# Optimization experiments

Measured on AMD Instinct MI355X. Metric: run time of the kernel, lower is better.

## Reference

```python
import jax, jax.numpy as jnp
import numpy as np

NODELEN = 394
N_NODES = 50000
N_EDGES = 200000
IN_DIM = 2 * NODELEN  # 788
H2 = 192
EMB = 128


def setup_inputs() -> dict:
    key = jax.random.key(0)
    ks = jax.random.split(key, 12)
    inp = {
        'features': jax.random.normal(ks[0], (N_NODES, NODELEN), dtype=jnp.float32),
        'src': jax.random.randint(ks[1], (N_EDGES,), 0, N_NODES),
        'dst': jax.random.randint(ks[2], (N_EDGES,), 0, N_NODES),
        # AutoEncoder params (Linear weights stored as [in, out])
        'W_enc1': jax.random.normal(ks[3], (IN_DIM, H2), dtype=jnp.float32) / np.sqrt(IN_DIM),
        'b_enc1': jnp.zeros((H2,), dtype=jnp.float32),
        'W_enc3': jax.random.normal(ks[4], (H2, EMB), dtype=jnp.float32) / np.sqrt(H2),
        'b_enc3': jnp.zeros((EMB,), dtype=jnp.float32),
        'W_dec1': jax.random.normal(ks[5], (EMB, H2), dtype=jnp.float32) / np.sqrt(EMB),
        'b_dec1': jnp.zeros((H2,), dtype=jnp.float32),
        'W_dec3': jax.random.normal(ks[6], (H2, IN_DIM), dtype=jnp.float32) / np.sqrt(H2),
        'b_dec3': jnp.zeros((IN_DIM,), dtype=jnp.float32),
    }
    return inp


def _segment_mean(msgs, dst, inv_deg, n):
    # msgs: [E, F] gathered neighbor features; mean over incoming edges per node
    return jax.ops.segment_sum(msgs, dst, num_segments=n) * inv_deg


def reference(features, src, dst, W_enc1, b_enc1, W_enc3, b_enc3,
              W_dec1, b_dec1, W_dec3, b_dec3):
    n = features.shape[0]
    ones = jnp.ones(src.shape[0], dtype=features.dtype)
    deg = jax.ops.segment_sum(ones, dst, num_segments=n)
    # nodes with no neighbors fall back to the zero dummy vector (as in source)
    inv_deg = (1.0 / jnp.maximum(deg, 1.0))[:, None]

    # depth-1 aggregation: mean of raw neighbor features, then feat[0] := 0
    h1 = _segment_mean(features[src], dst, inv_deg, n)
    h1 = h1.at[:, 0].set(0.0)
    # depth-2 aggregation: mean of depth-1 aggregates of neighbors, feat[0] := 0
    h2 = _segment_mean(h1[src], dst, inv_deg, n)
    h2 = h2.at[:, 0].set(0.0)

    # concatenated embedding with positions 0 and NODELEN zeroed
    emb = jnp.concatenate([features, h2], axis=1)  # [N, 788]
    emb = emb.at[:, 0].set(0.0).at[:, NODELEN].set(0.0)

    # AutoEncoder forward (dropout is identity at inference)
    x = jax.nn.relu(emb @ W_enc1 + b_enc1)
    encoded = x @ W_enc3 + b_enc3
    y = jax.nn.relu(encoded @ W_dec1 + b_dec1)
    decoded = y @ W_dec3 + b_dec3
    return encoded, decoded, emb
```

## Files before the change

### kernel.cpp

```cpp
#include <hip/hip_runtime.h>
#include <hip/hip_bf16.h>

#define NODELEN 394
#define IN_DIM 788
#define H2DIM 192
#define EMBDIM 128
#define NCHUNK 197

typedef __attribute__((ext_vector_type(4))) float f32x4;
typedef __attribute__((ext_vector_type(8))) short bfrag;

static __device__ __forceinline__ unsigned short f2bf(float f) {
    union { float f; unsigned u; } v; v.f = f;
    unsigned r = v.u + 0x7FFFu + ((v.u >> 16) & 1u);
    return (unsigned short)(r >> 16);
}
static __device__ __forceinline__ float bf2f(unsigned short h) {
    union { unsigned u; float f; } v; v.u = ((unsigned)h) << 16;
    return v.f;
}


__global__ void count_deg(const int* __restrict__ dst, int* __restrict__ deg, int e) {
    int i = blockIdx.x * blockDim.x + threadIdx.x;
    if (i < e) atomicAdd(&deg[dst[i]], 1);
}

__global__ void block_sum(const int* __restrict__ deg, int* __restrict__ bsum, int n) {
    __shared__ int s[256];
    int t = threadIdx.x;
    int i = blockIdx.x * 256 + t;
    s[t] = (i < n) ? deg[i] : 0;
    __syncthreads();
    for (int d = 128; d > 0; d >>= 1) {
        if (t < d) s[t] += s[t + d];
        __syncthreads();
    }
    if (t == 0) bsum[blockIdx.x] = s[0];
}

__global__ void scan_bsums(int* bsum, int nb) {
    __shared__ int s[256];
    int t = threadIdx.x;
    int x0 = (t < nb) ? bsum[t] : 0;
    s[t] = x0;
    __syncthreads();
    for (int d = 1; d < 256; d <<= 1) {
        int u = (t >= d) ? s[t - d] : 0;
        __syncthreads();
        s[t] += u;
        __syncthreads();
    }
    if (t < nb) bsum[t] = s[t] - x0;
}

__global__ void block_scan(const int* __restrict__ deg, const int* __restrict__ boff,
                           int* __restrict__ rowstart, int* __restrict__ cursor,
                           float* __restrict__ inv, int n) {
    __shared__ int s[256];
    int t = threadIdx.x;
    int i = blockIdx.x * 256 + t;
    int x0 = (i < n) ? deg[i] : 0;
    s[t] = x0;
    __syncthreads();
    for (int d = 1; d < 256; d <<= 1) {
        int u = (t >= d) ? s[t - d] : 0;
        __syncthreads();
        s[t] += u;
        __syncthreads();
    }
    if (i < n) {
        int r = boff[blockIdx.x] + s[t] - x0;
        rowstart[i] = r;
        cursor[i] = r;
        inv[i] = 1.0f / fmaxf((float)x0, 1.0f);
    }
}

__global__ void fill_edges(const int* __restrict__ src, const int* __restrict__ dst,
                           int* __restrict__ cursor, int* __restrict__ elist, int e) {
    int i = blockIdx.x * blockDim.x + threadIdx.x;
    if (i < e) {
        int p = atomicAdd(&cursor[dst[i]], 1);
        elist[p] = src[i];
    }
}


__global__ __launch_bounds__(256) void gather1(
        const float* __restrict__ feat, const int* __restrict__ rowstart,
        const int* __restrict__ deg, const float* __restrict__ inv,
        const int* __restrict__ elist, unsigned short* __restrict__ h1) {
    const int node = blockIdx.x;
    const int c = threadIdx.x;
    if (c >= NCHUNK) return;
    const int beg = rowstart[node];
    const int dc = deg[node];
    const float s = inv[node];
    const size_t off = (size_t)c * 2;

    float ax = 0.f, ay = 0.f, bx = 0.f, by = 0.f;
    float cx = 0.f, cy = 0.f, dx = 0.f, dy = 0.f;
    int j = 0;
    for (; j + 3 < dc; j += 4) {
        int n0 = elist[beg + j], n1 = elist[beg + j + 1];
        int n2 = elist[beg + j + 2], n3 = elist[beg + j + 3];
        float2 v0 = *(const float2*)(feat + (size_t)n0 * NODELEN + off);
        float2 v1 = *(const float2*)(feat + (size_t)n1 * NODELEN + off);
        float2 v2 = *(const float2*)(feat + (size_t)n2 * NODELEN + off);
        float2 v3 = *(const float2*)(feat + (size_t)n3 * NODELEN + off);
        ax += v0.x; ay += v0.y; bx += v1.x; by += v1.y;
        cx += v2.x; cy += v2.y; dx += v3.x; dy += v3.y;
    }
    for (; j < dc; ++j) {
        int n0 = elist[beg + j];
        float2 v0 = *(const float2*)(feat + (size_t)n0 * NODELEN + off);
        ax += v0.x; ay += v0.y;
    }
    float fx = (ax + bx + cx + dx) * s;
    float fy = (ay + by + cy + dy) * s;
    if (c == 0) fx = 0.f;
    unsigned out = ((unsigned)f2bf(fy) << 16) | (unsigned)f2bf(fx);
    *(unsigned*)(h1 + (size_t)node * NODELEN + off) = out;
}

__global__ __launch_bounds__(256) void gather2_emb(
        const float* __restrict__ feat, const unsigned* __restrict__ h1,
        const int* __restrict__ rowstart, const int* __restrict__ deg,
        const float* __restrict__ inv, const int* __restrict__ elist,
        float* __restrict__ emb) {
    const int node = blockIdx.x;
    const int c = threadIdx.x;
    if (c >= NCHUNK) return;
    const int beg = rowstart[node];
    const int dc = deg[node];
    const float s = inv[node];

    float ax = 0.f, ay = 0.f, bx = 0.f, by = 0.f;
    float cx = 0.f, cy = 0.f, dx = 0.f, dy = 0.f;
    int j = 0;
    for (; j + 3 < dc; j += 4) {
        int n0 = elist[beg + j], n1 = elist[beg + j + 1];
        int n2 = elist[beg + j + 2], n3 = elist[beg + j + 3];
        unsigned u0 = h1[(size_t)n0 * NCHUNK + c];
        unsigned u1 = h1[(size_t)n1 * NCHUNK + c];
        unsigned u2 = h1[(size_t)n2 * NCHUNK + c];
        unsigned u3 = h1[(size_t)n3 * NCHUNK + c];
        ax += bf2f((unsigned short)u0); ay += bf2f((unsigned short)(u0 >> 16));
        bx += bf2f((unsigned short)u1); by += bf2f((unsigned short)(u1 >> 16));
        cx += bf2f((unsigned short)u2); cy += bf2f((unsigned short)(u2 >> 16));
        dx += bf2f((unsigned short)u3); dy += bf2f((unsigned short)(u3 >> 16));
    }
    for (; j < dc; ++j) {
        int n0 = elist[beg + j];
        unsigned u0 = h1[(size_t)n0 * NCHUNK + c];
        ax += bf2f((unsigned short)u0); ay += bf2f((unsigned short)(u0 >> 16));
    }
    float hx = (ax + bx + cx + dx) * s;
    float hy = (ay + by + cy + dy) * s;

    const float* fr = feat + (size_t)node * NODELEN;
    float* er = emb + (size_t)node * IN_DIM;
    float2 fv = *(const float2*)(fr + c * 2);
    if (c == 0) { fv.x = 0.f; hx = 0.f; }
    *(float2*)(er + c * 2) = fv;
    float2 hv; hv.x = hx; hv.y = hy;
    *(float2*)(er + NODELEN + c * 2) = hv;
}

__device__ __forceinline__ void tr_one(const float* W, unsigned short* Wt,
                                       int K, int N, int Kp, int idx) {
    int nrow = idx / Kp, k = idx - nrow * Kp;
    Wt[idx] = (k < K) ? f2bf(W[(size_t)k * N + nrow]) : (unsigned short)0;
}

#define T1E (192 * 800)
#define T2E (128 * 192)
#define T3E (192 * 128)
#define T4E (788 * 192)

__global__ void transpose_all(const float* __restrict__ W1, unsigned short* __restrict__ Wt1,
                              const float* __restrict__ W2, unsigned short* __restrict__ Wt2,
                              const float* __restrict__ W3, unsigned short* __restrict__ Wt3,
                              const float* __restrict__ W4, unsigned short* __restrict__ Wt4) {
    int idx = blockIdx.x * 256 + threadIdx.x;
    if (idx < T1E) { tr_one(W1, Wt1, IN_DIM, H2DIM, 800, idx); return; }
    idx -= T1E;
    if (idx < T2E) { tr_one(W2, Wt2, H2DIM, EMBDIM, 192, idx); return; }
    idx -= T2E;
    if (idx < T3E) { tr_one(W3, Wt3, EMBDIM, H2DIM, 128, idx); return; }
    idx -= T3E;
    if (idx < T4E) { tr_one(W4, Wt4, H2DIM, IN_DIM, 192, idx); return; }
}

static __device__ __forceinline__ int bs_addr(int r, int s) {
    return r * 32 + ((s ^ ((r >> 1) & 3)) << 3);
}
static __device__ __forceinline__ int xy_base(int r, int s) {
    int ph = (s & 24) | ((s ^ r) & 7);
    return r * 192 + (ph << 3);
}
static __device__ __forceinline__ int xy_addr_s(int r, int col) { return xy_base(r, col >> 3) + (col & 7); }
static __device__ __forceinline__ int en_base(int r, int s) {
    int ph = (s & 8) | ((s ^ r) & 7);
    return r * 128 + (ph << 3);
}
static __device__ __forceinline__ int en_addr_s(int r, int col) { return en_base(r, col >> 3) + (col & 7); }

static __device__ __forceinline__ unsigned short f2bf_fast(float f) {
    __hip_bfloat16 h = __float2bfloat16(f);
    union { __hip_bfloat16 h; unsigned short u; } c; c.h = h; return c.u;
}

struct A8 { float4 a, b; };

static __device__ __forceinline__ void load_a(A8 out[2], const float* __restrict__ emb,
                                              int m0, int wm, int lr, int lk, int M, int kt) {
    int c = kt * 32 + lk * 8;
    #pragma unroll
    for (int i = 0; i < 2; ++i) {
        int gm = m0 + wm * 32 + i * 16 + lr;
        const float* rp = emb + (size_t)gm * IN_DIM;
        bool v = gm < M;
        if (v && c + 8 <= IN_DIM) {
            out[i].a = *(const float4*)(rp + c);
            out[i].b = *(const float4*)(rp + c + 4);
        } else {
            float t[8];
            #pragma unroll
            for (int q = 0; q < 8; ++q) t[q] = (v && c + q < IN_DIM) ? rp[c + q] : 0.f;
            out[i].a = make_float4(t[0], t[1], t[2], t[3]);
            out[i].b = make_float4(t[4], t[5], t[6], t[7]);
        }
    }
}

static __device__ __forceinline__ bfrag cvt_a(const A8& x) {
    union { unsigned short u[8]; bfrag v; } pk;
    pk.u[0] = f2bf_fast(x.a.x); pk.u[1] = f2bf_fast(x.a.y);
    pk.u[2] = f2bf_fast(x.a.z); pk.u[3] = f2bf_fast(x.a.w);
    pk.u[4] = f2bf_fast(x.b.x); pk.u[5] = f2bf_fast(x.b.y);
    pk.u[6] = f2bf_fast(x.b.z); pk.u[7] = f2bf_fast(x.b.w);
    return pk.v;
}

__global__ __launch_bounds__(256, 3) void mlp_fused(
    const float* __restrict__ emb,
    const unsigned short* __restrict__ Wt1,
    const unsigned short* __restrict__ Wt2,
    const unsigned short* __restrict__ Wt3,
    const unsigned short* __restrict__ Wt4,
    const float* __restrict__ b1, const float* __restrict__ b2,
    const float* __restrict__ b3, const float* __restrict__ b4,
    float* __restrict__ encoded, float* __restrict__ decoded, int M)
{
    __shared__ unsigned short Bs[192 * 32];
    __shared__ unsigned short XY[64 * 192];
    __shared__ unsigned short EN[64 * 128];

    const int tid = threadIdx.x;
    const int wid = tid >> 6, l = tid & 63;
    const int wm = wid >> 1, wn = wid & 1;
    const int lr = l & 15, lk = l >> 4;
    const int m0 = blockIdx.x * 64;
    const bfrag zf = {0, 0, 0, 0, 0, 0, 0, 0};

    const int r0 = tid >> 2, s0 = tid & 3;
    const int r1 = (tid + 256) >> 2;
    const int r2 = (tid + 512) >> 2;
    const int bw0 = bs_addr(r0, s0);
    const int bw1 = bs_addr(r1, s0);
    const int bw2 = bs_addr(r2, s0);
    int brd6[6], brd4[4];
    #pragma unroll
    for (int j = 0; j < 6; ++j) brd6[j] = bs_addr(wn * 96 + j * 16 + lr, lk);
    #pragma unroll
    for (int j = 0; j < 4; ++j) brd4[j] = bs_addr(wn * 64 + j * 16 + lr, lk);

    {
        f32x4 acc1[2][6];
        #pragma unroll
        for (int i = 0; i < 2; ++i)
            #pragma unroll
            for (int j = 0; j < 6; ++j) acc1[i][j] = (f32x4){0.f, 0.f, 0.f, 0.f};

        A8 aC[2], aN[2];
        bfrag bC[3], bN[3];
        load_a(aC, emb, m0, wm, lr, lk, M, 0);
        bC[0] = *(const bfrag*)(Wt1 + (size_t)r0 * 800 + s0 * 8);
        bC[1] = *(const bfrag*)(Wt1 + (size_t)r1 * 800 + s0 * 8);
        bC[2] = *(const bfrag*)(Wt1 + (size_t)r2 * 800 + s0 * 8);

        #pragma unroll 5
        for (int kt = 0; kt < 25; ++kt) {
            *(bfrag*)&Bs[bw0] = bC[0];
            *(bfrag*)&Bs[bw1] = bC[1];
            *(bfrag*)&Bs[bw2] = bC[2];
            if (kt < 24) {
                int k0 = (kt + 1) * 32;
                load_a(aN, emb, m0, wm, lr, lk, M, kt + 1);
                bN[0] = *(const bfrag*)(Wt1 + (size_t)r0 * 800 + k0 + s0 * 8);
                bN[1] = *(const bfrag*)(Wt1 + (size_t)r1 * 800 + k0 + s0 * 8);
                bN[2] = *(const bfrag*)(Wt1 + (size_t)r2 * 800 + k0 + s0 * 8);
            }
            __syncthreads();
            bfrag af0 = cvt_a(aC[0]), af1 = cvt_a(aC[1]);
            bfrag bf[6];
            #pragma unroll
            for (int j = 0; j < 6; ++j) bf[j] = *(const bfrag*)&Bs[brd6[j]];
            #pragma unroll
            for (int j = 0; j < 6; ++j) {
                acc1[0][j] = __builtin_amdgcn_mfma_f32_16x16x32_bf16(af0, bf[j], acc1[0][j], 0, 0, 0);
                acc1[1][j] = __builtin_amdgcn_mfma_f32_16x16x32_bf16(af1, bf[j], acc1[1][j], 0, 0, 0);
            }
            __syncthreads();
            if (kt < 24) {
                aC[0] = aN[0]; aC[1] = aN[1];
                bC[0] = bN[0]; bC[1] = bN[1]; bC[2] = bN[2];
            }
        }

        float bv[6];
        #pragma unroll
        for (int j = 0; j < 6; ++j) bv[j] = b1[wn * 96 + j * 16 + lr];
        #pragma unroll
        for (int i = 0; i < 2; ++i)
            #pragma unroll
            for (int j = 0; j < 6; ++j)
                #pragma unroll
                for (int r = 0; r < 4; ++r) {
                    int m = wm * 32 + i * 16 + lk * 4 + r;
                    int n1 = wn * 96 + j * 16 + lr;
                    XY[xy_addr_s(m, n1)] = f2bf_fast(fmaxf(acc1[i][j][r] + bv[j], 0.f));
                }
    }

    bfrag c3[3], n3[3];
    {
        bfrag c2[2], n2[2];
        c2[0] = *(const bfrag*)(Wt2 + (size_t)r0 * 192 + s0 * 8);
        c2[1] = *(const bfrag*)(Wt2 + (size_t)r1 * 192 + s0 * 8);
        f32x4 acc2[2][4];
        #pragma unroll
        for (int i = 0; i < 2; ++i)
            #pragma unroll
            for (int j = 0; j < 4; ++j) acc2[i][j] = (f32x4){0.f, 0.f, 0.f, 0.f};

        #pragma unroll
        for (int kt = 0; kt < 6; ++kt) {
            *(bfrag*)&Bs[bw0] = c2[0];
            *(bfrag*)&Bs[bw1] = c2[1];
            if (kt < 5) {
                int k0 = (kt + 1) * 32;
                n2[0] = *(const bfrag*)(Wt2 + (size_t)r0 * 192 + k0 + s0 * 8);
                n2[1] = *(const bfrag*)(Wt2 + (size_t)r1 * 192 + k0 + s0 * 8);
            } else {
                c3[0] = *(const bfrag*)(Wt3 + (size_t)r0 * 128 + s0 * 8);
                c3[1] = *(const bfrag*)(Wt3 + (size_t)r1 * 128 + s0 * 8);
                c3[2] = *(const bfrag*)(Wt3 + (size_t)r2 * 128 + s0 * 8);
            }
            __syncthreads();
            bfrag af[2];
            #pragma unroll
            for (int i = 0; i < 2; ++i)
                af[i] = *(const bfrag*)&XY[xy_base(wm * 32 + i * 16 + lr, kt * 4 + lk)];
            bfrag bf[4];
            #pragma unroll
            for (int j = 0; j < 4; ++j) bf[j] = *(const bfrag*)&Bs[brd4[j]];
            #pragma unroll
            for (int i = 0; i < 2; ++i)
                #pragma unroll
                for (int j = 0; j < 4; ++j)
                    acc2[i][j] = __builtin_amdgcn_mfma_f32_16x16x32_bf16(af[i], bf[j], acc2[i][j], 0, 0, 0);
            __syncthreads();
            if (kt < 5) { c2[0] = n2[0]; c2[1] = n2[1]; }
        }

        float bv[4];
        #pragma unroll
        for (int j = 0; j < 4; ++j) bv[j] = b2[wn * 64 + j * 16 + lr];
        #pragma unroll
        for (int i = 0; i < 2; ++i)
            #pragma unroll
            for (int j = 0; j < 4; ++j)
                #pragma unroll
                for (int r = 0; r < 4; ++r) {
                    int m = wm * 32 + i * 16 + lk * 4 + r;
                    int nn = wn * 64 + j * 16 + lr;
                    float v = acc2[i][j][r] + bv[j];
                    int gm = m0 + m;
                    if (gm < M) encoded[(size_t)gm * EMBDIM + nn] = v;
                    EN[en_addr_s(m, nn)] = f2bf_fast(v);
                }
    }

    bfrag c4[2], n4[2];
    {
        f32x4 acc3[2][6];
        #pragma unroll
        for (int i = 0; i < 2; ++i)
            #pragma unroll
            for (int j = 0; j < 6; ++j) acc3[i][j] = (f32x4){0.f, 0.f, 0.f, 0.f};

        #pragma unroll
        for (int kt = 0; kt < 4; ++kt) {
            *(bfrag*)&Bs[bw0] = c3[0];
            *(bfrag*)&Bs[bw1] = c3[1];
            *(bfrag*)&Bs[bw2] = c3[2];
            if (kt < 3) {
                int k0 = (kt + 1) * 32;
                n3[0] = *(const bfrag*)(Wt3 + (size_t)r0 * 128 + k0 + s0 * 8);
                n3[1] = *(const bfrag*)(Wt3 + (size_t)r1 * 128 + k0 + s0 * 8);
                n3[2] = *(const bfrag*)(Wt3 + (size_t)r2 * 128 + k0 + s0 * 8);
            } else {
                c4[0] = *(const bfrag*)(Wt4 + (size_t)r0 * 192 + s0 * 8);
                c4[1] = *(const bfrag*)(Wt4 + (size_t)r1 * 192 + s0 * 8);
            }
            __syncthreads();
            bfrag af[2];
            #pragma unroll
            for (int i = 0; i < 2; ++i)
                af[i] = *(const bfrag*)&EN[en_base(wm * 32 + i * 16 + lr, kt * 4 + lk)];
            bfrag bf[6];
            #pragma unroll
            for (int j = 0; j < 6; ++j) bf[j] = *(const bfrag*)&Bs[brd6[j]];
            #pragma unroll
            for (int i = 0; i < 2; ++i)
                #pragma unroll
                for (int j = 0; j < 6; ++j)
                    acc3[i][j] = __builtin_amdgcn_mfma_f32_16x16x32_bf16(af[i], bf[j], acc3[i][j], 0, 0, 0);
            __syncthreads();
            if (kt < 3) { c3[0] = n3[0]; c3[1] = n3[1]; c3[2] = n3[2]; }
        }

        float bv[6];
        #pragma unroll
        for (int j = 0; j < 6; ++j) bv[j] = b3[wn * 96 + j * 16 + lr];
        #pragma unroll
        for (int i = 0; i < 2; ++i)
            #pragma unroll
            for (int j = 0; j < 6; ++j)
                #pragma unroll
                for (int r = 0; r < 4; ++r) {
                    int m = wm * 32 + i * 16 + lk * 4 + r;
                    int n3c = wn * 96 + j * 16 + lr;
                    XY[xy_addr_s(m, n3c)] = f2bf_fast(fmaxf(acc3[i][j][r] + bv[j], 0.f));
                }
    }

    {
        bfrag af4[6][2];
        for (int nc = 0; nc < 7; ++nc) {
            f32x4 acc4[2][4];
            #pragma unroll
            for (int i = 0; i < 2; ++i)
                #pragma unroll
                for (int j = 0; j < 4; ++j) acc4[i][j] = (f32x4){0.f, 0.f, 0.f, 0.f};

            #pragma unroll
            for (int kt = 0; kt < 6; ++kt) {
                *(bfrag*)&Bs[bw0] = c4[0];
                *(bfrag*)&Bs[bw1] = c4[1];
                {
                    int nn = (kt < 5) ? nc : nc + 1;
                    int nk = (kt < 5) ? (kt + 1) * 32 : 0;
                    if (nn < 7) {
                        int g0 = nn * 128 + r0, g1 = nn * 128 + r1;
                        n4[0] = (g0 < IN_DIM) ? *(const bfrag*)(Wt4 + (size_t)g0 * 192 + nk + s0 * 8) : zf;
                        n4[1] = (g1 < IN_DIM) ? *(const bfrag*)(Wt4 + (size_t)g1 * 192 + nk + s0 * 8) : zf;
                    }
                }
                __syncthreads();
                if (nc == 0 && kt == 0) {
                    #pragma unroll
                    for (int q = 0; q < 6; ++q)
                        #pragma unroll
                        for (int i = 0; i < 2; ++i)
                            af4[q][i] = *(const bfrag*)&XY[xy_base(wm * 32 + i * 16 + lr, q * 4 + lk)];
                }
                bfrag bf[4];
                #pragma unroll
                for (int j = 0; j < 4; ++j) bf[j] = *(const bfrag*)&Bs[brd4[j]];
                #pragma unroll
                for (int i = 0; i < 2; ++i)
                    #pragma unroll
                    for (int j = 0; j < 4; ++j)
                        acc4[i][j] = __builtin_amdgcn_mfma_f32_16x16x32_bf16(af4[kt][i], bf[j], acc4[i][j], 0, 0, 0);
                __syncthreads();
                c4[0] = n4[0]; c4[1] = n4[1];
            }

            float bv[4];
            #pragma unroll
            for (int j = 0; j < 4; ++j) {
                int nn = nc * 128 + wn * 64 + j * 16 + lr;
                bv[j] = (nn < IN_DIM) ? b4[nn] : 0.f;
            }
            #pragma unroll
            for (int i = 0; i < 2; ++i)
                #pragma unroll
                for (int j = 0; j < 4; ++j)
                    #pragma unroll
                    for (int r = 0; r < 4; ++r) {
                        int gm = m0 + wm * 32 + i * 16 + lk * 4 + r;
                        int nn = nc * 128 + wn * 64 + j * 16 + lr;
                        if (gm < M && nn < IN_DIM)
                            decoded[(size_t)gm * IN_DIM + nn] = acc4[i][j][r] + bv[j];
                    }
        }
    }
}


extern "C" void kernel_launch(void* const* d_in, const int* in_sizes, int n_in,
                              void* d_out, int out_size, void* d_ws, size_t ws_size,
                              hipStream_t stream) {
    const float* features = (const float*)d_in[0];
    const int*   src      = (const int*)d_in[1];
    const int*   dst      = (const int*)d_in[2];
    const float* W_enc1   = (const float*)d_in[3];
    const float* b_enc1   = (const float*)d_in[4];
    const float* W_enc3   = (const float*)d_in[5];
    const float* b_enc3   = (const float*)d_in[6];
    const float* W_dec1   = (const float*)d_in[7];
    const float* b_dec1   = (const float*)d_in[8];
    const float* W_dec3   = (const float*)d_in[9];
    const float* b_dec3   = (const float*)d_in[10];

    const int n = in_sizes[0] / NODELEN;
    const int e = in_sizes[1];

    float* encoded = (float*)d_out;
    float* decoded = encoded + (size_t)n * EMBDIM;
    float* emb     = decoded + (size_t)n * IN_DIM;

    char* ws = (char*)d_ws;
    unsigned short* h1  = (unsigned short*)(ws + 0);
    unsigned short* Wt1 = (unsigned short*)(ws + 40000000);
    unsigned short* Wt2 = (unsigned short*)(ws + 40400000);
    unsigned short* Wt3 = (unsigned short*)(ws + 40500000);
    unsigned short* Wt4 = (unsigned short*)(ws + 40600000);
    float* inv          = (float*)(ws + 41000000);
    int*   deg          = (int*)  (ws + 41200000);
    int*   rowstart     = (int*)  (ws + 41400000);
    int*   cursor       = (int*)  (ws + 41600000);
    int*   elist        = (int*)  (ws + 41800000);
    int*   bsum         = (int*)  (ws + 42600000);

    const int nb = (n + 255) / 256;
    const int eb = (e + 255) / 256;

    transpose_all<<<(T1E + T2E + T3E + T4E + 255) / 256, 256, 0, stream>>>(
        W_enc1, Wt1, W_enc3, Wt2, W_dec1, Wt3, W_dec3, Wt4);

    hipMemsetAsync(deg, 0, (size_t)n * sizeof(int), stream);
    count_deg<<<eb, 256, 0, stream>>>(dst, deg, e);
    block_sum<<<nb, 256, 0, stream>>>(deg, bsum, n);
    scan_bsums<<<1, 256, 0, stream>>>(bsum, nb);
    block_scan<<<nb, 256, 0, stream>>>(deg, bsum, rowstart, cursor, inv, n);
    fill_edges<<<eb, 256, 0, stream>>>(src, dst, cursor, elist, e);

    gather1<<<n, 256, 0, stream>>>(features, rowstart, deg, inv, elist, h1);
    gather2_emb<<<n, 256, 0, stream>>>(features, (const unsigned*)h1, rowstart, deg,
                                       inv, elist, emb);

    const int MB = (n + 63) / 64;
    mlp_fused<<<MB, 256, 0, stream>>>(emb, Wt1, Wt2, Wt3, Wt4,
                                      b_enc1, b_enc3, b_dec1, b_dec3,
                                      encoded, decoded, n);
}
```

Baseline: 353.1 us.

## Load MLP weight fragments directly from global memory instead of staging through LDS

Removes the shared-memory B tile and its double-buffered register prefetch in all four GEMM stages. Each wave now reads its MFMA B fragments straight from global (L2-resident) weights and preloads the A fragments from XY/EN once per stage. This drops most __syncthreads and the LDS write/read round trip and frees LDS for occupancy. In exchange, the prefetch that hid global latency is gone, and each of the two wave rows in a block fetches the same weight data, raising L1/L2 traffic.

```diff
diff --git a/kernel.cpp b/kernel.cpp
--- a/kernel.cpp
+++ b/kernel.cpp
@@ -193,9 +193,6 @@
     if (idx < T4E) { tr_one(W4, Wt4, H2DIM, IN_DIM, 192, idx); return; }
 }
 
-static __device__ __forceinline__ int bs_addr(int r, int s) {
-    return r * 32 + ((s ^ ((r >> 1) & 3)) << 3);
-}
 static __device__ __forceinline__ int xy_base(int r, int s) {
     int ph = (s & 24) | ((s ^ r) & 7);
     return r * 192 + (ph << 3);
@@ -254,7 +251,6 @@
     const float* __restrict__ b3, const float* __restrict__ b4,
     float* __restrict__ encoded, float* __restrict__ decoded, int M)
 {
-    __shared__ unsigned short Bs[192 * 32];
     __shared__ unsigned short XY[64 * 192];
     __shared__ unsigned short EN[64 * 128];
 
@@ -265,61 +261,32 @@
     const int m0 = blockIdx.x * 64;
     const bfrag zf = {0, 0, 0, 0, 0, 0, 0, 0};
 
-    const int r0 = tid >> 2, s0 = tid & 3;
-    const int r1 = (tid + 256) >> 2;
-    const int r2 = (tid + 512) >> 2;
-    const int bw0 = bs_addr(r0, s0);
-    const int bw1 = bs_addr(r1, s0);
-    const int bw2 = bs_addr(r2, s0);
-    int brd6[6], brd4[4];
-    #pragma unroll
-    for (int j = 0; j < 6; ++j) brd6[j] = bs_addr(wn * 96 + j * 16 + lr, lk);
-    #pragma unroll
-    for (int j = 0; j < 4; ++j) brd4[j] = bs_addr(wn * 64 + j * 16 + lr, lk);
-
     {
-        f32x4 acc1[2][6];
+        f32x4 acc[2][6];
         #pragma unroll
         for (int i = 0; i < 2; ++i)
             #pragma unroll
-            for (int j = 0; j < 6; ++j) acc1[i][j] = (f32x4){0.f, 0.f, 0.f, 0.f};
-
-        A8 aC[2], aN[2];
-        bfrag bC[3], bN[3];
-        load_a(aC, emb, m0, wm, lr, lk, M, 0);
-        bC[0] = *(const bfrag*)(Wt1 + (size_t)r0 * 800 + s0 * 8);
-        bC[1] = *(const bfrag*)(Wt1 + (size_t)r1 * 800 + s0 * 8);
-        bC[2] = *(const bfrag*)(Wt1 + (size_t)r2 * 800 + s0 * 8);
+            for (int j = 0; j < 6; ++j) acc[i][j] = (f32x4){0.f, 0.f, 0.f, 0.f};
+
+        const unsigned short* wp[6];
+        #pragma unroll
+        for (int j = 0; j < 6; ++j)
+            wp[j] = Wt1 + (size_t)(wn * 96 + j * 16 + lr) * 800 + lk * 8;
 
         #pragma unroll 5
         for (int kt = 0; kt < 25; ++kt) {
-            *(bfrag*)&Bs[bw0] = bC[0];
-            *(bfrag*)&Bs[bw1] = bC[1];
-            *(bfrag*)&Bs[bw2] = bC[2];
-            if (kt < 24) {
-                int k0 = (kt + 1) * 32;
-                load_a(aN, emb, m0, wm, lr, lk, M, kt + 1);
-                bN[0] = *(const bfrag*)(Wt1 + (size_t)r0 * 800 + k0 + s0 * 8);
-                bN[1] = *(const bfrag*)(Wt1 + (size_t)r1 * 800 + k0 + s0 * 8);
-                bN[2] = *(const bfrag*)(Wt1 + (size_t)r2 * 800 + k0 + s0 * 8);
-            }
-            __syncthreads();
-            bfrag af0 = cvt_a(aC[0]), af1 = cvt_a(aC[1]);
+            A8 a[2];
+            load_a(a, emb, m0, wm, lr, lk, M, kt);
             bfrag bf[6];
             #pragma unroll
-            for (int j = 0; j < 6; ++j) bf[j] = *(const bfrag*)&Bs[brd6[j]];
+            for (int j = 0; j < 6; ++j) bf[j] = *(const bfrag*)(wp[j] + kt * 32);
+            bfrag af0 = cvt_a(a[0]), af1 = cvt_a(a[1]);
             #pragma unroll
             for (int j = 0; j < 6; ++j) {
-                acc1[0][j] = __builtin_amdgcn_mfma_f32_16x16x32_bf16(af0, bf[j], acc1[0][j], 0, 0, 0);
-                acc1[1][j] = __builtin_amdgcn_mfma_f32_16x16x32_bf16(af1, bf[j], acc1[1][j], 0, 0, 0);
-            }
-            __syncthreads();
-            if (kt < 24) {
-                aC[0] = aN[0]; aC[1] = aN[1];
-                bC[0] = bN[0]; bC[1] = bN[1]; bC[2] = bN[2];
+                acc[0][j] = __builtin_amdgcn_mfma_f32_16x16x32_bf16(af0, bf[j], acc[0][j], 0, 0, 0);
+                acc[1][j] = __builtin_amdgcn_mfma_f32_16x16x32_bf16(af1, bf[j], acc[1][j], 0, 0, 0);
             }
         }
-
         float bv[6];
         #pragma unroll
         for (int j = 0; j < 6; ++j) bv[j] = b1[wn * 96 + j * 16 + lr];
@@ -331,51 +298,41 @@
                 for (int r = 0; r < 4; ++r) {
                     int m = wm * 32 + i * 16 + lk * 4 + r;
                     int n1 = wn * 96 + j * 16 + lr;
-                    XY[xy_addr_s(m, n1)] = f2bf_fast(fmaxf(acc1[i][j][r] + bv[j], 0.f));
+                    XY[xy_addr_s(m, n1)] = f2bf_fast(fmaxf(acc[i][j][r] + bv[j], 0.f));
                 }
     }
-
-    bfrag c3[3], n3[3];
+    __syncthreads();
+
     {
-        bfrag c2[2], n2[2];
-        c2[0] = *(const bfrag*)(Wt2 + (size_t)r0 * 192 + s0 * 8);
-        c2[1] = *(const bfrag*)(Wt2 + (size_t)r1 * 192 + s0 * 8);
-        f32x4 acc2[2][4];
+        bfrag af2[6][2];
+        #pragma unroll
+        for (int q = 0; q < 6; ++q)
+            #pragma unroll
+            for (int i = 0; i < 2; ++i)
+                af2[q][i] = *(const bfrag*)&XY[xy_base(wm * 32 + i * 16 + lr, q * 4 + lk)];
+
+        f32x4 acc[2][4];
         #pragma unroll
         for (int i = 0; i < 2; ++i)
             #pragma unroll
-            for (int j = 0; j < 4; ++j) acc2[i][j] = (f32x4){0.f, 0.f, 0.f, 0.f};
+            for (int j = 0; j < 4; ++j) acc[i][j] = (f32x4){0.f, 0.f, 0.f, 0.f};
+
+        const unsigned short* wp[4];
+        #pragma unroll
+        for (int j = 0; j < 4; ++j)
+            wp[j] = Wt2 + (size_t)(wn * 64 + j * 16 + lr) * 192 + lk * 8;
 
         #pragma unroll
         for (int kt = 0; kt < 6; ++kt) {
-            *(bfrag*)&Bs[bw0] = c2[0];
-            *(bfrag*)&Bs[bw1] = c2[1];
-            if (kt < 5) {
-                int k0 = (kt + 1) * 32;
-                n2[0] = *(const bfrag*)(Wt2 + (size_t)r0 * 192 + k0 + s0 * 8);
-                n2[1] = *(const bfrag*)(Wt2 + (size_t)r1 * 192 + k0 + s0 * 8);
-            } else {
-                c3[0] = *(const bfrag*)(Wt3 + (size_t)r0 * 128 + s0 * 8);
-                c3[1] = *(const bfrag*)(Wt3 + (size_t)r1 * 128 + s0 * 8);
-                c3[2] = *(const bfrag*)(Wt3 + (size_t)r2 * 128 + s0 * 8);
-            }
-            __syncthreads();
-            bfrag af[2];
-            #pragma unroll
-            for (int i = 0; i < 2; ++i)
-                af[i] = *(const bfrag*)&XY[xy_base(wm * 32 + i * 16 + lr, kt * 4 + lk)];
             bfrag bf[4];
             #pragma unroll
-            for (int j = 0; j < 4; ++j) bf[j] = *(const bfrag*)&Bs[brd4[j]];
+            for (int j = 0; j < 4; ++j) bf[j] = *(const bfrag*)(wp[j] + kt * 32);
             #pragma unroll
             for (int i = 0; i < 2; ++i)
                 #pragma unroll
                 for (int j = 0; j < 4; ++j)
-                    acc2[i][j] = __builtin_amdgcn_mfma_f32_16x16x32_bf16(af[i], bf[j], acc2[i][j], 0, 0, 0);
-            __syncthreads();
-            if (kt < 5) { c2[0] = n2[0]; c2[1] = n2[1]; }
+                    acc[i][j] = __builtin_amdgcn_mfma_f32_16x16x32_bf16(af2[kt][i], bf[j], acc[i][j], 0, 0, 0);
         }
-
         float bv[4];
         #pragma unroll
         for (int j = 0; j < 4; ++j) bv[j] = b2[wn * 64 + j * 16 + lr];
@@ -387,52 +344,44 @@
                 for (int r = 0; r < 4; ++r) {
                     int m = wm * 32 + i * 16 + lk * 4 + r;
                     int nn = wn * 64 + j * 16 + lr;
-                    float v = acc2[i][j][r] + bv[j];
+                    float v = acc[i][j][r] + bv[j];
                     int gm = m0 + m;
                     if (gm < M) encoded[(size_t)gm * EMBDIM + nn] = v;
                     EN[en_addr_s(m, nn)] = f2bf_fast(v);
                 }
     }
-
-    bfrag c4[2], n4[2];
+    __syncthreads();
+
     {
-        f32x4 acc3[2][6];
+        bfrag af3[4][2];
+        #pragma unroll
+        for (int q = 0; q < 4; ++q)
+            #pragma unroll
+            for (int i = 0; i < 2; ++i)
+                af3[q][i] = *(const bfrag*)&EN[en_base(wm * 32 + i * 16 + lr, q * 4 + lk)];
+
+        f32x4 acc[2][6];
         #pragma unroll
         for (int i = 0; i < 2; ++i)
             #pragma unroll
-            for (int j = 0; j < 6; ++j) acc3[i][j] = (f32x4){0.f, 0.f, 0.f, 0.f};
+            for (int j = 0; j < 6; ++j) acc[i][j] = (f32x4){0.f, 0.f, 0.f, 0.f};
+
+        const unsigned short* wp[6];
+        #pragma unroll
+        for (int j = 0; j < 6; ++j)
+            wp[j] = Wt3 + (size_t)(wn * 96 + j * 16 + lr) * 128 + lk * 8;
 
         #pragma unroll
         for (int kt = 0; kt < 4; ++kt) {
-            *(bfrag*)&Bs[bw0] = c3[0];
-            *(bfrag*)&Bs[bw1] = c3[1];
-            *(bfrag*)&Bs[bw2] = c3[2];
-            if (kt < 3) {
-                int k0 = (kt + 1) * 32;
-                n3[0] = *(const bfrag*)(Wt3 + (size_t)r0 * 128 + k0 + s0 * 8);
-                n3[1] = *(const bfrag*)(Wt3 + (size_t)r1 * 128 + k0 + s0 * 8);
-                n3[2] = *(const bfrag*)(Wt3 + (size_t)r2 * 128 + k0 + s0 * 8);
-            } else {
-                c4[0] = *(const bfrag*)(Wt4 + (size_t)r0 * 192 + s0 * 8);
-                c4[1] = *(const bfrag*)(Wt4 + (size_t)r1 * 192 + s0 * 8);
-            }
-            __syncthreads();
-            bfrag af[2];
-            #pragma unroll
-            for (int i = 0; i < 2; ++i)
-                af[i] = *(const bfrag*)&EN[en_base(wm * 32 + i * 16 + lr, kt * 4 + lk)];
             bfrag bf[6];
             #pragma unroll
-            for (int j = 0; j < 6; ++j) bf[j] = *(const bfrag*)&Bs[brd6[j]];
+            for (int j = 0; j < 6; ++j) bf[j] = *(const bfrag*)(wp[j] + kt * 32);
             #pragma unroll
             for (int i = 0; i < 2; ++i)
                 #pragma unroll
                 for (int j = 0; j < 6; ++j)
-                    acc3[i][j] = __builtin_amdgcn_mfma_f32_16x16x32_bf16(af[i], bf[j], acc3[i][j], 0, 0, 0);
-            __syncthreads();
-            if (kt < 3) { c3[0] = n3[0]; c3[1] = n3[1]; c3[2] = n3[2]; }
+                    acc[i][j] = __builtin_amdgcn_mfma_f32_16x16x32_bf16(af3[kt][i], bf[j], acc[i][j], 0, 0, 0);
         }
-
         float bv[6];
         #pragma unroll
         for (int j = 0; j < 6; ++j) bv[j] = b3[wn * 96 + j * 16 + lr];
@@ -443,57 +392,48 @@
                 #pragma unroll
                 for (int r = 0; r < 4; ++r) {
                     int m = wm * 32 + i * 16 + lk * 4 + r;
-                    int n3c = wn * 96 + j * 16 + lr;
-                    XY[xy_addr_s(m, n3c)] = f2bf_fast(fmaxf(acc3[i][j][r] + bv[j], 0.f));
+                    int nc = wn * 96 + j * 16 + lr;
+                    XY[xy_addr_s(m, nc)] = f2bf_fast(fmaxf(acc[i][j][r] + bv[j], 0.f));
                 }
     }
+    __syncthreads();
 
     {
         bfrag af4[6][2];
+        #pragma unroll
+        for (int q = 0; q < 6; ++q)
+            #pragma unroll
+            for (int i = 0; i < 2; ++i)
+                af4[q][i] = *(const bfrag*)&XY[xy_base(wm * 32 + i * 16 + lr, q * 4 + lk)];
+
         for (int nc = 0; nc < 7; ++nc) {
-            f32x4 acc4[2][4];
-            #pragma unroll
-            for (int i = 0; i < 2; ++i)
-                #pragma unroll
-                for (int j = 0; j < 4; ++j) acc4[i][j] = (f32x4){0.f, 0.f, 0.f, 0.f};
-
+            f32x4 acc[2][4];
+            #pragma unroll
+            for (int i = 0; i < 2; ++i)
+                #pragma unroll
+                for (int j = 0; j < 4; ++j) acc[i][j] = (f32x4){0.f, 0.f, 0.f, 0.f};
+
+            const int colb = nc * 128 + wn * 64 + lr;
             #pragma unroll
             for (int kt = 0; kt < 6; ++kt) {
-                *(bfrag*)&Bs[bw0] = c4[0];
-                *(bfrag*)&Bs[bw1] = c4[1];
-                {
-                    int nn = (kt < 5) ? nc : nc + 1;
-                    int nk = (kt < 5) ? (kt + 1) * 32 : 0;
-                    if (nn < 7) {
-                        int g0 = nn * 128 + r0, g1 = nn * 128 + r1;
-                        n4[0] = (g0 < IN_DIM) ? *(const bfrag*)(Wt4 + (size_t)g0 * 192 + nk + s0 * 8) : zf;
-                        n4[1] = (g1 < IN_DIM) ? *(const bfrag*)(Wt4 + (size_t)g1 * 192 + nk + s0 * 8) : zf;
-                    }
+                bfrag bf[4];
+                #pragma unroll
+                for (int j = 0; j < 4; ++j) {
+                    int row = colb + j * 16;
+                    bf[j] = (row < IN_DIM)
+                        ? *(const bfrag*)(Wt4 + (size_t)row * 192 + kt * 32 + lk * 8) : zf;
                 }
-                __syncthreads();
-                if (nc == 0 && kt == 0) {
-                    #pragma unroll
-                    for (int q = 0; q < 6; ++q)
-                        #pragma unroll
-                        for (int i = 0; i < 2; ++i)
-                            af4[q][i] = *(const bfrag*)&XY[xy_base(wm * 32 + i * 16 + lr, q * 4 + lk)];
-                }
-                bfrag bf[4];
-                #pragma unroll
-                for (int j = 0; j < 4; ++j) bf[j] = *(const bfrag*)&Bs[brd4[j]];
                 #pragma unroll
                 for (int i = 0; i < 2; ++i)
                     #pragma unroll
                     for (int j = 0; j < 4; ++j)
-                        acc4[i][j] = __builtin_amdgcn_mfma_f32_16x16x32_bf16(af4[kt][i], bf[j], acc4[i][j], 0, 0, 0);
-                __syncthreads();
-                c4[0] = n4[0]; c4[1] = n4[1];
+                        acc[i][j] = __builtin_amdgcn_mfma_f32_16x16x32_bf16(af4[kt][i], bf[j], acc[i][j], 0, 0, 0);
             }
 
             float bv[4];
             #pragma unroll
             for (int j = 0; j < 4; ++j) {
-                int nn = nc * 128 + wn * 64 + j * 16 + lr;
+                int nn = colb + j * 16;
                 bv[j] = (nn < IN_DIM) ? b4[nn] : 0.f;
             }
             #pragma unroll
@@ -503,9 +443,9 @@
                     #pragma unroll
                     for (int r = 0; r < 4; ++r) {
                         int gm = m0 + wm * 32 + i * 16 + lk * 4 + r;
-                        int nn = nc * 128 + wn * 64 + j * 16 + lr;
+                        int nn = colb + j * 16;
                         if (gm < M && nn < IN_DIM)
-                            decoded[(size_t)gm * IN_DIM + nn] = acc4[i][j][r] + bv[j];
+                            decoded[(size_t)gm * IN_DIM + nn] = acc[i][j][r] + bv[j];
                     }
         }
     }
```

Result: slower. 415.3 us (+17.6%).
